# Optimization experiments

Hardware: AMD Instinct MI355X
Metric: run time of the kernel (lower is better)

The kernel has to match this reference:

```python
import jax, jax.numpy as jnp
import numpy as np

NEG_BIG = -9e15
ALPHA = 0.2  # LeakyReLU negative slope


def setup_inputs() -> dict:
    key = jax.random.key(0)
    k1, k2, k3, k4 = jax.random.split(key, 4)
    B, N, Fin, Fout = 4, 2048, 128, 128
    h = jax.random.normal(k1, (B, N, Fin), dtype=jnp.float32)
    adj = jax.random.randint(k2, (N, N), 0, 2, dtype=jnp.int32)
    W = jax.random.normal(k3, (Fin, Fout), dtype=jnp.float32) * 0.1
    a = jax.random.normal(k4, (2 * Fout, 1), dtype=jnp.float32) * 0.1
    return {"h": h, "adj": adj, "W": W, "a": a}


def reference(h, adj, W, a):
    # Wh: [B, N, Fout]
    Wh = jnp.einsum('bnf,fo->bno', h, W)
    Fout = W.shape[1]
    a1 = a[:Fout, 0]   # attends to source i
    a2 = a[Fout:, 0]   # attends to target j
    # Decomposed form of leakyrelu(cat([Wh_i, Wh_j]) @ a):
    # e_ij = leakyrelu(a1.Wh_i + a2.Wh_j)  -> [B, N, N]
    f1 = Wh @ a1  # [B, N]
    f2 = Wh @ a2  # [B, N]
    e = jax.nn.leaky_relu(f1[:, :, None] + f2[:, None, :], negative_slope=ALPHA)
    attention = jnp.where(adj[None, :, :] > 0, e, jnp.float32(NEG_BIG))
    attention = jax.nn.softmax(attention, axis=2)
    # dropout is identity in eval mode
    h_prime = jnp.einsum('bij,bjo->bio', attention, Wh)
    return h_prime
```

## Files before the change

kernel.cpp:

```cpp
#include <hip/hip_runtime.h>

#define BB 4
#define NN 2048
#define FF 128
#define ALPHA 0.2f
#define NEG_BIG -9000000000000000.0f
#define SHIFT_C 16.0f

typedef short bf16x8 __attribute__((ext_vector_type(8)));
typedef short bf16x4 __attribute__((ext_vector_type(4)));
typedef float f32x4 __attribute__((ext_vector_type(4)));

__device__ inline short f2bf(float f) {
    union { float f; unsigned u; } v; v.f = f;
    unsigned r = (v.u + 0x7FFFu + ((v.u >> 16) & 1u)) >> 16;
    return (short)r;
}
__device__ inline float bf2f(short s) {
    union { float f; unsigned u; } v;
    v.u = ((unsigned)(unsigned short)s) << 16;
    return v.f;
}

__global__ __launch_bounds__(256) void k_wh(const float* __restrict__ h,
                                            const float* __restrict__ W,
                                            const float* __restrict__ a,
                                            short* __restrict__ WhHiT,
                                            short* __restrict__ WhLoT,
                                            float* __restrict__ f1,
                                            float* __restrict__ f2) {
    __shared__ float Wa[2 * FF];
    __shared__ float hs[32 * 128];
    int tid = threadIdx.x;
    int r0 = blockIdx.x * 32;

    {
        int fin = tid & 127;
        const float* av = (tid < 128) ? a : (a + FF);
        const float* wr = W + (size_t)fin * FF;
        float s = 0.f;
        for (int o = 0; o < FF; o += 4) {
            float4 wv = *(const float4*)(wr + o);
            float4 avv = *(const float4*)(av + o);
            s += wv.x * avv.x + wv.y * avv.y + wv.z * avv.z + wv.w * avv.w;
        }
        Wa[(tid < 128 ? 0 : FF) + fin] = s;
    }
    {
        const float4* src = (const float4*)(h + (size_t)r0 * FF);
        float4* dst = (float4*)hs;
#pragma unroll
        for (int it = 0; it < 4; ++it)
            dst[it * 256 + tid] = src[it * 256 + tid];
    }
    __syncthreads();

    {
        int w = tid >> 6, lane = tid & 63;
        float wa1_0 = Wa[lane], wa1_1 = Wa[lane + 64];
        float wa2_0 = Wa[FF + lane], wa2_1 = Wa[FF + lane + 64];
        for (int rr = 0; rr < 8; ++rr) {
            int rloc = w * 8 + rr;
            int row = r0 + rloc;
            float x0 = hs[rloc * FF + lane], x1 = hs[rloc * FF + lane + 64];
            float s1 = x0 * wa1_0 + x1 * wa1_1;
            float s2 = x0 * wa2_0 + x1 * wa2_1;
#pragma unroll
            for (int m = 32; m >= 1; m >>= 1) {
                s1 += __shfl_xor(s1, m, 64);
                s2 += __shfl_xor(s2, m, 64);
            }
            if (lane == 0) { f1[row] = s1; f2[row] = s2; }
        }
    }

    int f4 = (tid & 31) * 4;
    int rg = tid >> 5;
    float acc[4][4];
#pragma unroll
    for (int rr = 0; rr < 4; ++rr)
#pragma unroll
        for (int cc = 0; cc < 4; ++cc) acc[rr][cc] = 0.f;

    for (int k0 = 0; k0 < FF; k0 += 4) {
        float4 wv[4];
#pragma unroll
        for (int kk = 0; kk < 4; ++kk)
            wv[kk] = *(const float4*)(W + (size_t)(k0 + kk) * FF + f4);
        float4 hv[4];
#pragma unroll
        for (int rr = 0; rr < 4; ++rr)
            hv[rr] = *(const float4*)(hs + (rg * 4 + rr) * FF + k0);
#pragma unroll
        for (int rr = 0; rr < 4; ++rr) {
            float hk[4] = {hv[rr].x, hv[rr].y, hv[rr].z, hv[rr].w};
#pragma unroll
            for (int kk = 0; kk < 4; ++kk) {
                acc[rr][0] += hk[kk] * wv[kk].x;
                acc[rr][1] += hk[kk] * wv[kk].y;
                acc[rr][2] += hk[kk] * wv[kk].z;
                acc[rr][3] += hk[kk] * wv[kk].w;
            }
        }
    }
    int rloc = r0 + rg * 4;
    int b = rloc >> 11;
    int j = rloc & (NN - 1);
#pragma unroll
    for (int cc = 0; cc < 4; ++cc) {
        bf16x4 ph, pl;
#pragma unroll
        for (int k = 0; k < 4; ++k) {
            float v = acc[k][cc];
            short hi = f2bf(v);
            ph[k] = hi;
            pl[k] = f2bf(v - bf2f(hi));
        }
        size_t off = ((size_t)(b * FF + f4 + cc)) * NN + j;
        *(bf16x4*)(WhHiT + off) = ph;
        *(bf16x4*)(WhLoT + off) = pl;
    }
}

__global__ __launch_bounds__(512) void k_attn(const short* __restrict__ WhHiT,
                                              const short* __restrict__ WhLoT,
                                              const int* __restrict__ adj,
                                              const float* __restrict__ f1,
                                              const float* __restrict__ f2,
                                              float* __restrict__ out) {
    __shared__ float obuf[4][2048];
    __shared__ float row_s[8][16];
    __shared__ float row_inv[16];

    int tid = threadIdx.x;
    int b = blockIdx.x >> 7;
    int i0 = (blockIdx.x & 127) * 16;
    int w = tid >> 6, lane = tid & 63;

    const float* f2b = f2 + b * NN;

    int r_a = lane & 15;
    int kg = lane >> 4;
    int i = i0 + r_a;
    float f1i = f1[b * NN + i];
    const int* adjrow = adj + (size_t)i * NN;
    const short* baseH = WhHiT + ((size_t)b * FF + r_a) * NN;
    const short* baseL = WhLoT + ((size_t)b * FF + r_a) * NN;

    f32x4 acc[8];
#pragma unroll
    for (int n = 0; n < 8; ++n)
#pragma unroll
        for (int q = 0; q < 4; ++q) acc[n][q] = 0.f;
    float sp = 0.f;

    int jb0 = w * 256 + kg * 8;
    int4 pa0 = *(const int4*)(adjrow + jb0);
    int4 pa1 = *(const int4*)(adjrow + jb0 + 4);
    float4 pq0 = *(const float4*)(f2b + jb0);
    float4 pq1 = *(const float4*)(f2b + jb0 + 4);

    for (int c = 0; c < 8; ++c) {
        int jb = w * 256 + c * 32 + kg * 8;
        int4 a0 = pa0, a1 = pa1;
        float4 q0 = pq0, q1 = pq1;
        int jb_n = w * 256 + ((c + 1) & 7) * 32 + kg * 8;
        pa0 = *(const int4*)(adjrow + jb_n);
        pa1 = *(const int4*)(adjrow + jb_n + 4);
        pq0 = *(const float4*)(f2b + jb_n);
        pq1 = *(const float4*)(f2b + jb_n + 4);

        int av[8] = {a0.x, a0.y, a0.z, a0.w, a1.x, a1.y, a1.z, a1.w};
        float qv[8] = {q0.x, q0.y, q0.z, q0.w, q1.x, q1.y, q1.z, q1.w};
        bf16x8 afrag;
#pragma unroll
        for (int t = 0; t < 8; ++t) {
            float x = f1i + qv[t];
            x = x > 0.f ? x : ALPHA * x;
            x = av[t] > 0 ? x : NEG_BIG;
            short pb = f2bf(__expf(x - SHIFT_C));
            sp += bf2f(pb);
            afrag[t] = pb;
        }
        const short* bh = baseH + jb;
        const short* bl = baseL + jb;
#pragma unroll
        for (int n = 0; n < 8; ++n) {
            bf16x8 fh = *(const bf16x8*)(bh + (size_t)n * 16 * NN);
            acc[n] = __builtin_amdgcn_mfma_f32_16x16x32_bf16(afrag, fh, acc[n], 0, 0, 0);
            bf16x8 fl = *(const bf16x8*)(bl + (size_t)n * 16 * NN);
            acc[n] = __builtin_amdgcn_mfma_f32_16x16x32_bf16(afrag, fl, acc[n], 0, 0, 0);
        }
    }

    sp += __shfl_xor(sp, 16, 64);
    sp += __shfl_xor(sp, 32, 64);
    if (lane < 16) row_s[w][lane] = sp;

    if (w >= 4) {
#pragma unroll
        for (int n = 0; n < 8; ++n)
#pragma unroll
            for (int q = 0; q < 4; ++q)
                obuf[w - 4][(kg * 4 + q) * FF + n * 16 + r_a] = acc[n][q];
    }
    __syncthreads();
    if (tid < 16)
        row_inv[tid] = 1.0f / (row_s[0][tid] + row_s[1][tid] + row_s[2][tid] + row_s[3][tid] +
                               row_s[4][tid] + row_s[5][tid] + row_s[6][tid] + row_s[7][tid]);
    if (w < 4) {
#pragma unroll
        for (int n = 0; n < 8; ++n)
#pragma unroll
            for (int q = 0; q < 4; ++q)
                acc[n][q] += obuf[w][(kg * 4 + q) * FF + n * 16 + r_a];
    }
    __syncthreads();
    if (w == 2 || w == 3) {
#pragma unroll
        for (int n = 0; n < 8; ++n)
#pragma unroll
            for (int q = 0; q < 4; ++q)
                obuf[w - 2][(kg * 4 + q) * FF + n * 16 + r_a] = acc[n][q];
    }
    __syncthreads();
    if (w < 2) {
#pragma unroll
        for (int n = 0; n < 8; ++n)
#pragma unroll
            for (int q = 0; q < 4; ++q)
                acc[n][q] += obuf[w][(kg * 4 + q) * FF + n * 16 + r_a];
    }
    __syncthreads();
    if (w == 1) {
#pragma unroll
        for (int n = 0; n < 8; ++n)
#pragma unroll
            for (int q = 0; q < 4; ++q)
                obuf[1][(kg * 4 + q) * FF + n * 16 + r_a] = acc[n][q];
    }
    __syncthreads();
    if (w == 0) {
#pragma unroll
        for (int n = 0; n < 8; ++n)
#pragma unroll
            for (int q = 0; q < 4; ++q) {
                int o = (kg * 4 + q) * FF + n * 16 + r_a;
                obuf[0][o] = acc[n][q] + obuf[1][o];
            }
    }
    __syncthreads();

    {
        int e = tid * 4;
        int row = e >> 7;
        float inv = row_inv[row];
        float4 v = *(const float4*)&obuf[0][e];
        float4 o;
        o.x = v.x * inv; o.y = v.y * inv; o.z = v.z * inv; o.w = v.w * inv;
        *(float4*)(out + ((size_t)b * NN + i0 + row) * FF + (e & 127)) = o;
    }
}

extern "C" void kernel_launch(void* const* d_in, const int* in_sizes, int n_in,
                              void* d_out, int out_size, void* d_ws, size_t ws_size,
                              hipStream_t stream) {
    const float* h   = (const float*)d_in[0];
    const int*   adj = (const int*)d_in[1];
    const float* W   = (const float*)d_in[2];
    const float* a   = (const float*)d_in[3];
    float* out = (float*)d_out;

    short* WhHiT = (short*)d_ws;
    short* WhLoT = WhHiT + (size_t)BB * FF * NN;
    float* f1 = (float*)(WhLoT + (size_t)BB * FF * NN);
    float* f2 = f1 + (size_t)BB * NN;

    k_wh<<<(BB * NN) / 32, 256, 0, stream>>>(h, W, a, WhHiT, WhLoT, f1, f2);
    k_attn<<<BB * (NN / 16), 512, 0, stream>>>(WhHiT, WhLoT, adj, f1, f2, out);
}
```

Baseline: 152.0 us.

## Bit-pack adjacency, pad transposed Wh rows, and halve k_wh tile

Adds a pre-pass kernel that packs the int32 adjacency matrix into a bitmask using wave ballots, so the attention kernel reads 32x less adjacency data and each wave needs only two int4 loads per row. The transposed bf16 Wh hi/lo buffers get a padded row stride of 2176 instead of 2048, which should spread accesses across memory channels and cache sets. The Wh projection kernel now handles 16 rows per block instead of 32, doubling the block count, and the attention kernel gains an occupancy hint and a fully unrolled chunk loop. The cost is one extra kernel launch plus a full read of the adjacency matrix on every call.

```diff
diff --git a/kernel.cpp b/kernel.cpp
--- a/kernel.cpp
+++ b/kernel.cpp
@@ -3,12 +3,12 @@
 #define BB 4
 #define NN 2048
 #define FF 128
+#define NP 2176
 #define ALPHA 0.2f
 #define NEG_BIG -9000000000000000.0f
 #define SHIFT_C 16.0f
 
 typedef short bf16x8 __attribute__((ext_vector_type(8)));
-typedef short bf16x4 __attribute__((ext_vector_type(4)));
 typedef float f32x4 __attribute__((ext_vector_type(4)));
 
 __device__ inline short f2bf(float f) {
@@ -20,6 +20,19 @@
     union { float f; unsigned u; } v;
     v.u = ((unsigned)(unsigned short)s) << 16;
     return v.f;
+}
+
+__global__ __launch_bounds__(256) void k_pack(const int* __restrict__ adj,
+                                              unsigned* __restrict__ adjp) {
+    int w = threadIdx.x >> 6, lane = threadIdx.x & 63;
+    int row = blockIdx.x * 4 + w;
+    const int* ar = adj + (size_t)row * NN;
+    for (int it = 0; it < 32; ++it) {
+        int v = ar[it * 64 + lane];
+        unsigned long long mask = __ballot(v > 0);
+        if (lane == 0) adjp[row * 64 + it * 2] = (unsigned)mask;
+        if (lane == 1) adjp[row * 64 + it * 2 + 1] = (unsigned)(mask >> 32);
+    }
 }
 
 __global__ __launch_bounds__(256) void k_wh(const float* __restrict__ h,
@@ -30,9 +43,9 @@
                                             float* __restrict__ f1,
                                             float* __restrict__ f2) {
     __shared__ float Wa[2 * FF];
-    __shared__ float hs[32 * 128];
+    __shared__ float hs[16 * 128];
     int tid = threadIdx.x;
-    int r0 = blockIdx.x * 32;
+    int r0 = blockIdx.x * 16;
 
     {
         int fin = tid & 127;
@@ -49,9 +62,8 @@
     {
         const float4* src = (const float4*)(h + (size_t)r0 * FF);
         float4* dst = (float4*)hs;
-#pragma unroll
-        for (int it = 0; it < 4; ++it)
-            dst[it * 256 + tid] = src[it * 256 + tid];
+        dst[tid] = src[tid];
+        dst[256 + tid] = src[256 + tid];
     }
     __syncthreads();
 
@@ -59,8 +71,8 @@
         int w = tid >> 6, lane = tid & 63;
         float wa1_0 = Wa[lane], wa1_1 = Wa[lane + 64];
         float wa2_0 = Wa[FF + lane], wa2_1 = Wa[FF + lane + 64];
-        for (int rr = 0; rr < 8; ++rr) {
-            int rloc = w * 8 + rr;
+        for (int rr = 0; rr < 4; ++rr) {
+            int rloc = w * 4 + rr;
             int row = r0 + rloc;
             float x0 = hs[rloc * FF + lane], x1 = hs[rloc * FF + lane + 64];
             float s1 = x0 * wa1_0 + x1 * wa1_1;
@@ -76,9 +88,9 @@
 
     int f4 = (tid & 31) * 4;
     int rg = tid >> 5;
-    float acc[4][4];
-#pragma unroll
-    for (int rr = 0; rr < 4; ++rr)
+    float acc[2][4];
+#pragma unroll
+    for (int rr = 0; rr < 2; ++rr)
 #pragma unroll
         for (int cc = 0; cc < 4; ++cc) acc[rr][cc] = 0.f;
 
@@ -87,12 +99,12 @@
 #pragma unroll
         for (int kk = 0; kk < 4; ++kk)
             wv[kk] = *(const float4*)(W + (size_t)(k0 + kk) * FF + f4);
-        float4 hv[4];
-#pragma unroll
-        for (int rr = 0; rr < 4; ++rr)
-            hv[rr] = *(const float4*)(hs + (rg * 4 + rr) * FF + k0);
-#pragma unroll
-        for (int rr = 0; rr < 4; ++rr) {
+        float4 hv[2];
+#pragma unroll
+        for (int rr = 0; rr < 2; ++rr)
+            hv[rr] = *(const float4*)(hs + (rg * 2 + rr) * FF + k0);
+#pragma unroll
+        for (int rr = 0; rr < 2; ++rr) {
             float hk[4] = {hv[rr].x, hv[rr].y, hv[rr].z, hv[rr].w};
 #pragma unroll
             for (int kk = 0; kk < 4; ++kk) {
@@ -103,31 +115,26 @@
             }
         }
     }
-    int rloc = r0 + rg * 4;
+    int rloc = r0 + rg * 2;
     int b = rloc >> 11;
     int j = rloc & (NN - 1);
 #pragma unroll
     for (int cc = 0; cc < 4; ++cc) {
-        bf16x4 ph, pl;
-#pragma unroll
-        for (int k = 0; k < 4; ++k) {
-            float v = acc[k][cc];
-            short hi = f2bf(v);
-            ph[k] = hi;
-            pl[k] = f2bf(v - bf2f(hi));
-        }
-        size_t off = ((size_t)(b * FF + f4 + cc)) * NN + j;
-        *(bf16x4*)(WhHiT + off) = ph;
-        *(bf16x4*)(WhLoT + off) = pl;
-    }
-}
-
-__global__ __launch_bounds__(512) void k_attn(const short* __restrict__ WhHiT,
-                                              const short* __restrict__ WhLoT,
-                                              const int* __restrict__ adj,
-                                              const float* __restrict__ f1,
-                                              const float* __restrict__ f2,
-                                              float* __restrict__ out) {
+        float v0 = acc[0][cc], v1 = acc[1][cc];
+        short h0 = f2bf(v0), h1 = f2bf(v1);
+        short l0 = f2bf(v0 - bf2f(h0)), l1 = f2bf(v1 - bf2f(h1));
+        size_t off = (size_t)(b * FF + f4 + cc) * NP + j;
+        *(short2*)(WhHiT + off) = make_short2(h0, h1);
+        *(short2*)(WhLoT + off) = make_short2(l0, l1);
+    }
+}
+
+__global__ __launch_bounds__(512, 4) void k_attn(const short* __restrict__ WhHiT,
+                                                 const short* __restrict__ WhLoT,
+                                                 const unsigned* __restrict__ adjp,
+                                                 const float* __restrict__ f1,
+                                                 const float* __restrict__ f2,
+                                                 float* __restrict__ out) {
     __shared__ float obuf[4][2048];
     __shared__ float row_s[8][16];
     __shared__ float row_inv[16];
@@ -143,9 +150,14 @@
     int kg = lane >> 4;
     int i = i0 + r_a;
     float f1i = f1[b * NN + i];
-    const int* adjrow = adj + (size_t)i * NN;
-    const short* baseH = WhHiT + ((size_t)b * FF + r_a) * NN;
-    const short* baseL = WhLoT + ((size_t)b * FF + r_a) * NN;
+    const short* baseH = WhHiT + ((size_t)b * FF + r_a) * NP;
+    const short* baseL = WhLoT + ((size_t)b * FF + r_a) * NP;
+
+    const int4* aprow = (const int4*)(adjp + (size_t)i * 64);
+    int4 pw0 = aprow[w * 2];
+    int4 pw1 = aprow[w * 2 + 1];
+    unsigned wordv[8] = {(unsigned)pw0.x, (unsigned)pw0.y, (unsigned)pw0.z, (unsigned)pw0.w,
+                         (unsigned)pw1.x, (unsigned)pw1.y, (unsigned)pw1.z, (unsigned)pw1.w};
 
     f32x4 acc[8];
 #pragma unroll
@@ -155,40 +167,37 @@
     float sp = 0.f;
 
     int jb0 = w * 256 + kg * 8;
-    int4 pa0 = *(const int4*)(adjrow + jb0);
-    int4 pa1 = *(const int4*)(adjrow + jb0 + 4);
     float4 pq0 = *(const float4*)(f2b + jb0);
     float4 pq1 = *(const float4*)(f2b + jb0 + 4);
 
+#pragma unroll
     for (int c = 0; c < 8; ++c) {
         int jb = w * 256 + c * 32 + kg * 8;
-        int4 a0 = pa0, a1 = pa1;
         float4 q0 = pq0, q1 = pq1;
         int jb_n = w * 256 + ((c + 1) & 7) * 32 + kg * 8;
-        pa0 = *(const int4*)(adjrow + jb_n);
-        pa1 = *(const int4*)(adjrow + jb_n + 4);
         pq0 = *(const float4*)(f2b + jb_n);
         pq1 = *(const float4*)(f2b + jb_n + 4);
 
-        int av[8] = {a0.x, a0.y, a0.z, a0.w, a1.x, a1.y, a1.z, a1.w};
+        unsigned word = wordv[c] >> (kg * 8);
         float qv[8] = {q0.x, q0.y, q0.z, q0.w, q1.x, q1.y, q1.z, q1.w};
         bf16x8 afrag;
 #pragma unroll
         for (int t = 0; t < 8; ++t) {
             float x = f1i + qv[t];
             x = x > 0.f ? x : ALPHA * x;
-            x = av[t] > 0 ? x : NEG_BIG;
+            x = ((word >> t) & 1u) ? x : NEG_BIG;
             short pb = f2bf(__expf(x - SHIFT_C));
             sp += bf2f(pb);
             afrag[t] = pb;
         }
+
         const short* bh = baseH + jb;
         const short* bl = baseL + jb;
 #pragma unroll
         for (int n = 0; n < 8; ++n) {
-            bf16x8 fh = *(const bf16x8*)(bh + (size_t)n * 16 * NN);
+            bf16x8 fh = *(const bf16x8*)(bh + (size_t)n * 16 * NP);
             acc[n] = __builtin_amdgcn_mfma_f32_16x16x32_bf16(afrag, fh, acc[n], 0, 0, 0);
-            bf16x8 fl = *(const bf16x8*)(bl + (size_t)n * 16 * NN);
+            bf16x8 fl = *(const bf16x8*)(bl + (size_t)n * 16 * NP);
             acc[n] = __builtin_amdgcn_mfma_f32_16x16x32_bf16(afrag, fl, acc[n], 0, 0, 0);
         }
     }
@@ -272,10 +281,12 @@
     float* out = (float*)d_out;
 
     short* WhHiT = (short*)d_ws;
-    short* WhLoT = WhHiT + (size_t)BB * FF * NN;
-    float* f1 = (float*)(WhLoT + (size_t)BB * FF * NN);
+    short* WhLoT = WhHiT + (size_t)BB * FF * NP;
+    float* f1 = (float*)(WhLoT + (size_t)BB * FF * NP);
     float* f2 = f1 + (size_t)BB * NN;
-
-    k_wh<<<(BB * NN) / 32, 256, 0, stream>>>(h, W, a, WhHiT, WhLoT, f1, f2);
-    k_attn<<<BB * (NN / 16), 512, 0, stream>>>(WhHiT, WhLoT, adj, f1, f2, out);
-}
+    unsigned* adjp = (unsigned*)(f2 + (size_t)BB * NN);
+
+    k_pack<<<NN / 4, 256, 0, stream>>>(adj, adjp);
+    k_wh<<<(BB * NN) / 16, 256, 0, stream>>>(h, W, a, WhHiT, WhLoT, f1, f2);
+    k_attn<<<BB * (NN / 16), 512, 0, stream>>>(WhHiT, WhLoT, adjp, f1, f2, out);
+}
```

Result: slower. 165.6 us (+8.9%).
